# Performance work log

Hardware: AMD Instinct MI355X
Metric: run time of the kernel (lower is better)

The kernel has to match this reference:

```python
import jax, jax.numpy as jnp
import numpy as np

ALPHA = 0.01
BETA = 3e-05
OUT_H, OUT_W = 256, 256
KSIZE, SIGMA = 5, 4.0


def _gaussian_kernel2d(ks=KSIZE, sigma=SIGMA):
    x = jnp.arange(ks, dtype=jnp.float32) - (ks - 1) / 2.0
    g = jnp.exp(-(x * x) / (2.0 * sigma * sigma))
    g = g / g.sum()
    return jnp.outer(g, g)  # [ks, ks]


def _gaussian_blur(maps):
    # maps: [B, H, W]; reflect padding + depthwise 5x5 gaussian (kornia-style GaussianBlur2d)
    k = _gaussian_kernel2d()[None, None]  # [1,1,5,5]
    p = KSIZE // 2
    x = jnp.pad(maps[:, None], ((0, 0), (0, 0), (p, p), (p, p)), mode='reflect')
    y = jax.lax.conv_general_dilated(x, k, (1, 1), 'VALID')
    return y[:, 0]


def _resize_bilinear_align_corners(x, oh, ow):
    # x: [B, h, w] -> [B, oh, ow], torch F.interpolate(mode='bilinear', align_corners=True)
    B, h, w = x.shape
    ys = jnp.linspace(0.0, h - 1.0, oh)
    xs = jnp.linspace(0.0, w - 1.0, ow)
    y0 = jnp.floor(ys).astype(jnp.int32)
    x0 = jnp.floor(xs).astype(jnp.int32)
    y1 = jnp.minimum(y0 + 1, h - 1)
    x1 = jnp.minimum(x0 + 1, w - 1)
    fy = (ys - y0.astype(ys.dtype))[:, None]  # [oh,1]
    fx = (xs - x0.astype(xs.dtype))[None, :]  # [1,ow]
    a = x[:, y0][:, :, x0]
    b = x[:, y0][:, :, x1]
    c = x[:, y1][:, :, x0]
    d = x[:, y1][:, :, x1]
    top = a * (1.0 - fx) + b * fx
    bot = c * (1.0 - fx) + d * fx
    return top * (1.0 - fy) + bot * fy


def setup_inputs() -> dict:
    key = jax.random.key(0)
    k0, k1, k2 = jax.random.split(key, 3)
    B = 256
    return {
        'out0': jax.random.normal(k0, (B, 64, 64), jnp.float32),
        'out1': jax.random.normal(k1, (B, 32, 32), jnp.float32),
        'out2': jax.random.normal(k2, (B, 16, 16), jnp.float32),
    }


def reference(out0, out1, out2):
    outputs = [out0, out1, out2]
    B = out0.shape[0]
    # per-sample max of each scale -> softmax-weighted selection of per-sample weight
    max_vals = jnp.stack([o.reshape(B, -1).max(axis=1) for o in outputs], axis=1)  # [B,3]
    probs = jax.nn.softmax(max_vals, axis=1)
    mask = probs > probs.mean(axis=1, keepdims=True)  # probs > prob_mean
    cnt = mask.sum(axis=1)
    sel_mean = (max_vals * mask).sum(axis=1) / jnp.maximum(cnt, 1)
    total_weights = jnp.where(cnt > 0, jnp.maximum(sel_mean * ALPHA, BETA), BETA)  # [B]
    # multi-scale fusion: bilinear(align_corners=True) upsample to (256,256) and sum
    maps = _resize_bilinear_align_corners(out0, OUT_H, OUT_W)
    maps = maps + _resize_bilinear_align_corners(out1, OUT_H, OUT_W)
    maps = maps + _resize_bilinear_align_corners(out2, OUT_H, OUT_W)
    # gaussian blur then per-sample score. torch takes topk(k=f(total_weights)).values[0],
    # and topk values are sorted descending, so values[0] == max (k / total_weights drop out).
    blurred = _gaussian_blur(maps)
    scores = blurred.reshape(B, -1).max(axis=1)
    del total_weights  # only influenced the (unused) top-k size in the original
    return scores[:, None], maps
```

## Files before the change

kernel.cpp:

```cpp
#include <hip/hip_runtime.h>
#include <math.h>


static constexpr int W  = 256;
static constexpr int QH = 4;
static constexpr int ROWS = 64;

__device__ __forceinline__ int reflect256(int i) {
    if (i < 0) i = -i;
    if (i > 255) i = 510 - i;
    return i;
}

template<int H>
__device__ __forceinline__ float sample_direct(const float* __restrict__ base,
                                               int ry, int x0, int x1, float fx) {
    int   iy = ry * (H - 1);
    int   y0 = iy / 255;
    float fy = (float)(iy - 255 * y0) * (1.0f / 255.0f);
    int   y1 = min(y0 + 1, H - 1);
    float a = base[y0 * H + x0];
    float b = base[y0 * H + x1];
    float c = base[y1 * H + x0];
    float d = base[y1 * H + x1];
    float top = a + fx * (b - a);
    float bot = c + fx * (d - c);
    return top + fy * (bot - top);
}

__global__ __launch_bounds__(256, 4) void fused_kernel(
    const float* __restrict__ in0,
    const float* __restrict__ in1,
    const float* __restrict__ in2,
    float* __restrict__ part,
    float* __restrict__ maps)
{
    const int t   = threadIdx.x;
    const int bid = blockIdx.x;
    const int b   = bid >> 2;
    const int r0  = (bid & 3) * ROWS;

    __shared__ float s0[64 * 64];
    __shared__ float s1[32 * 32];
    __shared__ float s2[16 * 16];
    __shared__ float vsm[16][W];
    __shared__ float red[4];

    {
        const float4* g0 = (const float4*)(in0 + (size_t)b * 4096);
        const float4* g1 = (const float4*)(in1 + (size_t)b * 1024);
        const float4* g2 = (const float4*)(in2 + (size_t)b * 256);
        float4* l0 = (float4*)s0;
        float4* l1 = (float4*)s1;
        float4* l2 = (float4*)s2;
#pragma unroll
        for (int i = 0; i < 4; ++i) l0[t + i * 256] = g0[t + i * 256];
        l1[t] = g1[t];
        if (t < 64) l2[t] = g2[t];
    }
    __syncthreads();

    const float inv255 = 1.0f / 255.0f;
    int ix0 = t * 63; int x00 = ix0 / 255; float fx0 = (float)(ix0 - 255 * x00) * inv255; int x01 = min(x00 + 1, 63);
    int ix1 = t * 31; int x10 = ix1 / 255; float fx1 = (float)(ix1 - 255 * x10) * inv255; int x11 = min(x10 + 1, 31);
    int ix2 = t * 15; int x20 = ix2 / 255; float fx2 = (float)(ix2 - 255 * x20) * inv255; int x21 = min(x20 + 1, 15);

    auto xr0 = [&](int y) { float a = s0[y * 64 + x00]; float bb = s0[y * 64 + x01]; return a + fx0 * (bb - a); };
    auto xr1 = [&](int y) { float a = s1[y * 32 + x10]; float bb = s1[y * 32 + x11]; return a + fx1 * (bb - a); };
    auto xr2 = [&](int y) { float a = s2[y * 16 + x20]; float bb = s2[y * 16 + x21]; return a + fx2 * (bb - a); };

    auto direct = [&](int rn) -> float {
        int ry = reflect256(rn);
        return sample_direct<64>(s0, ry, x00, x01, fx0)
             + sample_direct<32>(s1, ry, x10, x11, fx1)
             + sample_direct<16>(s2, ry, x20, x21, fx2);
    };

    const float e1 = expf(-1.0f / 32.0f);
    const float e2 = expf(-4.0f / 32.0f);
    const float nrm = 1.0f + 2.0f * e1 + 2.0f * e2;
    const float wc = 1.0f / nrm, wa = e1 / nrm, wb = e2 / nrm;

    float m0 = direct(r0 - 2);
    float m1 = direct(r0 - 1);
    float m2 = direct(r0);
    float m3 = direct(r0 + 1);
    float* __restrict__ mbase = maps + ((size_t)b * W) * W + t;
    mbase[(size_t)(r0) * W]     = m2;
    mbase[(size_t)(r0 + 1) * W] = m3;

    int iy;
    iy = (r0 + 2) * 63; int ya = iy / 255; int rem0 = iy - ya * 255;
    float rlo0 = xr0(ya), rhi0 = xr0(min(ya + 1, 63));
    iy = (r0 + 2) * 31; int yb = iy / 255; int rem1 = iy - yb * 255;
    float rlo1 = xr1(yb), rhi1 = xr1(min(yb + 1, 31));
    iy = (r0 + 2) * 15; int yc = iy / 255; int rem2 = iy - yc * 255;
    float rlo2 = xr2(yc), rhi2 = xr2(min(yc + 1, 15));

    const int qx = t & 63;
    const int c0 = qx * 4;
    const int rowbase = t >> 6;
    const int ca = max(c0 - 4, 0);
    const int cc = min(c0 + 4, 252);

    float gmax = -INFINITY;

    for (int i = 0; i < ROWS; ++i) {
        const int rn = r0 + 2 + i;
        float mnew;
        if (rn <= 255) {
            float v0 = rlo0 + (float)rem0 * inv255 * (rhi0 - rlo0);
            float v1 = rlo1 + (float)rem1 * inv255 * (rhi1 - rlo1);
            float v2 = rlo2 + (float)rem2 * inv255 * (rhi2 - rlo2);
            mnew = v0 + v1 + v2;
            rem0 += 63; if (rem0 >= 255) { rem0 -= 255; ya++; rlo0 = rhi0; rhi0 = xr0(min(ya + 1, 63)); }
            rem1 += 31; if (rem1 >= 255) { rem1 -= 255; yb++; rlo1 = rhi1; rhi1 = xr1(min(yb + 1, 31)); }
            rem2 += 15; if (rem2 >= 255) { rem2 -= 255; yc++; rlo2 = rhi2; rhi2 = xr2(min(yc + 1, 15)); }
        } else {
            mnew = direct(rn);
        }

        if (i < ROWS - 2) {
            mbase[(size_t)rn * W] = mnew;
        }

        vsm[i & 15][t] = wb * (m0 + mnew) + wa * (m1 + m3) + wc * m2;
        m0 = m1; m1 = m2; m2 = m3; m3 = mnew;

        if ((i & 15) == 15) {
            __syncthreads();
#pragma unroll
            for (int k = 0; k < 4; ++k) {
                const int row = rowbase + k * 4;
                const float4 Bv = *(const float4*)&vsm[row][c0];
                const float4 Av = *(const float4*)&vsm[row][ca];
                const float4 Cv = *(const float4*)&vsm[row][cc];
                const float a2 = (qx == 0)  ? Bv.z : Av.z;
                const float a3 = (qx == 0)  ? Bv.y : Av.w;
                const float c4 = (qx == 63) ? Bv.z : Cv.x;
                const float c5 = (qx == 63) ? Bv.y : Cv.y;
                float o0 = wc * Bv.x + wa * (a3 + Bv.y)   + wb * (a2 + Bv.z);
                float o1 = wc * Bv.y + wa * (Bv.x + Bv.z) + wb * (a3 + Bv.w);
                float o2 = wc * Bv.z + wa * (Bv.y + Bv.w) + wb * (Bv.x + c4);
                float o3 = wc * Bv.w + wa * (Bv.z + c4)   + wb * (Bv.y + c5);
                gmax = fmaxf(gmax, fmaxf(fmaxf(o0, o1), fmaxf(o2, o3)));
            }
            __syncthreads();
        }
    }

#pragma unroll
    for (int off = 32; off > 0; off >>= 1)
        gmax = fmaxf(gmax, __shfl_down(gmax, off));
    if ((t & 63) == 0) red[t >> 6] = gmax;
    __syncthreads();
    if (t == 0)
        part[bid] = fmaxf(fmaxf(red[0], red[1]), fmaxf(red[2], red[3]));
}

__global__ void reduce_kernel(const float* __restrict__ part,
                              float* __restrict__ scores, int B) {
    int i = blockIdx.x * blockDim.x + threadIdx.x;
    if (i < B) {
        float m = part[QH * i];
#pragma unroll
        for (int k = 1; k < QH; ++k) m = fmaxf(m, part[QH * i + k]);
        scores[i] = m;
    }
}

extern "C" void kernel_launch(void* const* d_in, const int* in_sizes, int n_in,
                              void* d_out, int out_size, void* d_ws, size_t ws_size,
                              hipStream_t stream) {
    const float* in0 = (const float*)d_in[0];
    const float* in1 = (const float*)d_in[1];
    const float* in2 = (const float*)d_in[2];
    const int B = in_sizes[0] / (64 * 64);

    float* scores = (float*)d_out;
    float* maps   = (float*)d_out + B;
    float* part   = (float*)d_ws;

    hipLaunchKernelGGL(fused_kernel, dim3(B * QH), dim3(256), 0, stream,
                       in0, in1, in2, part, maps);
    hipLaunchKernelGGL(reduce_kernel, dim3((B + 255) / 256), dim3(256), 0, stream,
                       part, scores, B);
}
```

Baseline: 100.4 us.

## Give each wavefront a 16-row strip with 4 columns per lane and shuffle-based blur

Re-partitions work so each wavefront handles 16 output rows and each lane computes 4 adjacent columns, writing maps with float4 stores. The horizontal blur pass now uses wavefront shuffles instead of a shared-memory staging buffer with block-wide barriers, which removes the vsm array and the __syncthreads inside the row loop. In exchange, each wavefront recomputes 4 halo rows directly, and each lane holds several 4-wide register arrays, which raises register pressure.

```diff
diff --git a/kernel.cpp b/kernel.cpp
--- a/kernel.cpp
+++ b/kernel.cpp
@@ -4,28 +4,11 @@
 
 static constexpr int W  = 256;
 static constexpr int QH = 4;
-static constexpr int ROWS = 64;
 
 __device__ __forceinline__ int reflect256(int i) {
     if (i < 0) i = -i;
     if (i > 255) i = 510 - i;
     return i;
-}
-
-template<int H>
-__device__ __forceinline__ float sample_direct(const float* __restrict__ base,
-                                               int ry, int x0, int x1, float fx) {
-    int   iy = ry * (H - 1);
-    int   y0 = iy / 255;
-    float fy = (float)(iy - 255 * y0) * (1.0f / 255.0f);
-    int   y1 = min(y0 + 1, H - 1);
-    float a = base[y0 * H + x0];
-    float b = base[y0 * H + x1];
-    float c = base[y1 * H + x0];
-    float d = base[y1 * H + x1];
-    float top = a + fx * (b - a);
-    float bot = c + fx * (d - c);
-    return top + fy * (bot - top);
 }
 
 __global__ __launch_bounds__(256, 4) void fused_kernel(
@@ -36,14 +19,17 @@
     float* __restrict__ maps)
 {
     const int t   = threadIdx.x;
+    const int q   = t & 63;
+    const int wv  = __builtin_amdgcn_readfirstlane(t >> 6);
     const int bid = blockIdx.x;
     const int b   = bid >> 2;
-    const int r0  = (bid & 3) * ROWS;
+    const int r0  = (bid & 3) * 64;
+    const int rw0 = r0 + wv * 16;
+    const int c0  = q * 4;
 
     __shared__ float s0[64 * 64];
     __shared__ float s1[32 * 32];
     __shared__ float s2[16 * 16];
-    __shared__ float vsm[16][W];
     __shared__ float red[4];
 
     {
@@ -61,98 +47,165 @@
     __syncthreads();
 
     const float inv255 = 1.0f / 255.0f;
-    int ix0 = t * 63; int x00 = ix0 / 255; float fx0 = (float)(ix0 - 255 * x00) * inv255; int x01 = min(x00 + 1, 63);
-    int ix1 = t * 31; int x10 = ix1 / 255; float fx1 = (float)(ix1 - 255 * x10) * inv255; int x11 = min(x10 + 1, 31);
-    int ix2 = t * 15; int x20 = ix2 / 255; float fx2 = (float)(ix2 - 255 * x20) * inv255; int x21 = min(x20 + 1, 15);
-
-    auto xr0 = [&](int y) { float a = s0[y * 64 + x00]; float bb = s0[y * 64 + x01]; return a + fx0 * (bb - a); };
-    auto xr1 = [&](int y) { float a = s1[y * 32 + x10]; float bb = s1[y * 32 + x11]; return a + fx1 * (bb - a); };
-    auto xr2 = [&](int y) { float a = s2[y * 16 + x20]; float bb = s2[y * 16 + x21]; return a + fx2 * (bb - a); };
-
-    auto direct = [&](int rn) -> float {
-        int ry = reflect256(rn);
-        return sample_direct<64>(s0, ry, x00, x01, fx0)
-             + sample_direct<32>(s1, ry, x10, x11, fx1)
-             + sample_direct<16>(s2, ry, x20, x21, fx2);
+    int x00[4]; float fx0[4];
+    int x10[4]; float fx1[4];
+    int x20[4]; float fx2[4];
+#pragma unroll
+    for (int k = 0; k < 4; ++k) {
+        const int c = c0 + k;
+        int ix = c * 63; x00[k] = ix / 255; fx0[k] = (float)(ix - 255 * x00[k]) * inv255;
+        ix = c * 31;     x10[k] = ix / 255; fx1[k] = (float)(ix - 255 * x10[k]) * inv255;
+        ix = c * 15;     x20[k] = ix / 255; fx2[k] = (float)(ix - 255 * x20[k]) * inv255;
+    }
+
+    auto xq0 = [&](int y, float* o) {
+        const float* row = s0 + y * 64;
+#pragma unroll
+        for (int k = 0; k < 4; ++k) {
+            int xa = x00[k], xb = min(xa + 1, 63);
+            float a = row[xa], bb = row[xb];
+            o[k] = a + fx0[k] * (bb - a);
+        }
+    };
+    auto xq1 = [&](int y, float* o) {
+        const float* row = s1 + y * 32;
+#pragma unroll
+        for (int k = 0; k < 4; ++k) {
+            int xa = x10[k], xb = min(xa + 1, 31);
+            float a = row[xa], bb = row[xb];
+            o[k] = a + fx1[k] * (bb - a);
+        }
+    };
+    auto xq2 = [&](int y, float* o) {
+        const float* row = s2 + y * 16;
+#pragma unroll
+        for (int k = 0; k < 4; ++k) {
+            int xa = x20[k], xb = min(xa + 1, 15);
+            float a = row[xa], bb = row[xb];
+            o[k] = a + fx2[k] * (bb - a);
+        }
+    };
+
+    auto direct4 = [&](int rn, float* o) {
+        const int ry = reflect256(rn);
+        int iy0 = ry * 63; int ya0 = iy0 / 255; float fya = (float)(iy0 - 255 * ya0) * inv255; int ya1 = min(ya0 + 1, 63);
+        int iy1 = ry * 31; int yb0 = iy1 / 255; float fyb = (float)(iy1 - 255 * yb0) * inv255; int yb1 = min(yb0 + 1, 31);
+        int iy2 = ry * 15; int yc0 = iy2 / 255; float fyc = (float)(iy2 - 255 * yc0) * inv255; int yc1 = min(yc0 + 1, 15);
+        const float* r0a = s0 + ya0 * 64; const float* r0b = s0 + ya1 * 64;
+        const float* r1a = s1 + yb0 * 32; const float* r1b = s1 + yb1 * 32;
+        const float* r2a = s2 + yc0 * 16; const float* r2b = s2 + yc1 * 16;
+#pragma unroll
+        for (int k = 0; k < 4; ++k) {
+            int xa = x00[k], xb = min(xa + 1, 63);
+            float a = r0a[xa], bv = r0a[xb], cv = r0b[xa], dv = r0b[xb];
+            float top = a + fx0[k] * (bv - a);
+            float bot = cv + fx0[k] * (dv - cv);
+            float v = top + fya * (bot - top);
+            xa = x10[k]; xb = min(xa + 1, 31);
+            a = r1a[xa]; bv = r1a[xb]; cv = r1b[xa]; dv = r1b[xb];
+            top = a + fx1[k] * (bv - a);
+            bot = cv + fx1[k] * (dv - cv);
+            v += top + fyb * (bot - top);
+            xa = x20[k]; xb = min(xa + 1, 15);
+            a = r2a[xa]; bv = r2a[xb]; cv = r2b[xa]; dv = r2b[xb];
+            top = a + fx2[k] * (bv - a);
+            bot = cv + fx2[k] * (dv - cv);
+            v += top + fyc * (bot - top);
+            o[k] = v;
+        }
     };
 
     const float e1 = expf(-1.0f / 32.0f);
     const float e2 = expf(-4.0f / 32.0f);
     const float nrm = 1.0f + 2.0f * e1 + 2.0f * e2;
-    const float wc = 1.0f / nrm, wa = e1 / nrm, wb = e2 / nrm;
-
-    float m0 = direct(r0 - 2);
-    float m1 = direct(r0 - 1);
-    float m2 = direct(r0);
-    float m3 = direct(r0 + 1);
-    float* __restrict__ mbase = maps + ((size_t)b * W) * W + t;
-    mbase[(size_t)(r0) * W]     = m2;
-    mbase[(size_t)(r0 + 1) * W] = m3;
-
-    int iy;
-    iy = (r0 + 2) * 63; int ya = iy / 255; int rem0 = iy - ya * 255;
-    float rlo0 = xr0(ya), rhi0 = xr0(min(ya + 1, 63));
-    iy = (r0 + 2) * 31; int yb = iy / 255; int rem1 = iy - yb * 255;
-    float rlo1 = xr1(yb), rhi1 = xr1(min(yb + 1, 31));
-    iy = (r0 + 2) * 15; int yc = iy / 255; int rem2 = iy - yc * 255;
-    float rlo2 = xr2(yc), rhi2 = xr2(min(yc + 1, 15));
-
-    const int qx = t & 63;
-    const int c0 = qx * 4;
-    const int rowbase = t >> 6;
-    const int ca = max(c0 - 4, 0);
-    const int cc = min(c0 + 4, 252);
+    const float gwc = 1.0f / nrm, gwa = e1 / nrm, gwb = e2 / nrm;
+
+    float m0[4], m1[4], m2[4], m3[4], mn[4];
+    direct4(rw0 - 2, m0);
+    direct4(rw0 - 1, m1);
+    direct4(rw0,     m2);
+    direct4(rw0 + 1, m3);
+
+    float* __restrict__ mpr = maps + ((size_t)b * W + (size_t)rw0) * W + c0;
+    *(float4*)(mpr)     = make_float4(m2[0], m2[1], m2[2], m2[3]);
+    *(float4*)(mpr + W) = make_float4(m3[0], m3[1], m3[2], m3[3]);
+
+    int iy, ya, yb, yc, rem0, rem1, rem2;
+    float rlo0[4], rhi0[4], rlo1[4], rhi1[4], rlo2[4], rhi2[4];
+    iy = (rw0 + 2) * 63; ya = iy / 255; rem0 = iy - 255 * ya; xq0(ya, rlo0); xq0(min(ya + 1, 63), rhi0);
+    iy = (rw0 + 2) * 31; yb = iy / 255; rem1 = iy - 255 * yb; xq1(yb, rlo1); xq1(min(yb + 1, 31), rhi1);
+    iy = (rw0 + 2) * 15; yc = iy / 255; rem2 = iy - 255 * yc; xq2(yc, rlo2); xq2(min(yc + 1, 15), rhi2);
 
     float gmax = -INFINITY;
 
-    for (int i = 0; i < ROWS; ++i) {
-        const int rn = r0 + 2 + i;
-        float mnew;
+#pragma unroll 4
+    for (int i = 0; i < 16; ++i) {
+        const int rn = rw0 + 2 + i;
         if (rn <= 255) {
-            float v0 = rlo0 + (float)rem0 * inv255 * (rhi0 - rlo0);
-            float v1 = rlo1 + (float)rem1 * inv255 * (rhi1 - rlo1);
-            float v2 = rlo2 + (float)rem2 * inv255 * (rhi2 - rlo2);
-            mnew = v0 + v1 + v2;
-            rem0 += 63; if (rem0 >= 255) { rem0 -= 255; ya++; rlo0 = rhi0; rhi0 = xr0(min(ya + 1, 63)); }
-            rem1 += 31; if (rem1 >= 255) { rem1 -= 255; yb++; rlo1 = rhi1; rhi1 = xr1(min(yb + 1, 31)); }
-            rem2 += 15; if (rem2 >= 255) { rem2 -= 255; yc++; rlo2 = rhi2; rhi2 = xr2(min(yc + 1, 15)); }
+            const float w0 = (float)rem0 * inv255;
+            const float w1 = (float)rem1 * inv255;
+            const float w2 = (float)rem2 * inv255;
+#pragma unroll
+            for (int k = 0; k < 4; ++k) {
+                float v0 = rlo0[k] + w0 * (rhi0[k] - rlo0[k]);
+                float v1 = rlo1[k] + w1 * (rhi1[k] - rlo1[k]);
+                float v2 = rlo2[k] + w2 * (rhi2[k] - rlo2[k]);
+                mn[k] = v0 + v1 + v2;
+            }
+            rem0 += 63;
+            if (rem0 >= 255) {
+                rem0 -= 255; ++ya;
+#pragma unroll
+                for (int k = 0; k < 4; ++k) rlo0[k] = rhi0[k];
+                xq0(min(ya + 1, 63), rhi0);
+            }
+            rem1 += 31;
+            if (rem1 >= 255) {
+                rem1 -= 255; ++yb;
+#pragma unroll
+                for (int k = 0; k < 4; ++k) rlo1[k] = rhi1[k];
+                xq1(min(yb + 1, 31), rhi1);
+            }
+            rem2 += 15;
+            if (rem2 >= 255) {
+                rem2 -= 255; ++yc;
+#pragma unroll
+                for (int k = 0; k < 4; ++k) rlo2[k] = rhi2[k];
+                xq2(min(yc + 1, 15), rhi2);
+            }
         } else {
-            mnew = direct(rn);
-        }
-
-        if (i < ROWS - 2) {
-            mbase[(size_t)rn * W] = mnew;
-        }
-
-        vsm[i & 15][t] = wb * (m0 + mnew) + wa * (m1 + m3) + wc * m2;
-        m0 = m1; m1 = m2; m2 = m3; m3 = mnew;
-
-        if ((i & 15) == 15) {
-            __syncthreads();
-#pragma unroll
-            for (int k = 0; k < 4; ++k) {
-                const int row = rowbase + k * 4;
-                const float4 Bv = *(const float4*)&vsm[row][c0];
-                const float4 Av = *(const float4*)&vsm[row][ca];
-                const float4 Cv = *(const float4*)&vsm[row][cc];
-                const float a2 = (qx == 0)  ? Bv.z : Av.z;
-                const float a3 = (qx == 0)  ? Bv.y : Av.w;
-                const float c4 = (qx == 63) ? Bv.z : Cv.x;
-                const float c5 = (qx == 63) ? Bv.y : Cv.y;
-                float o0 = wc * Bv.x + wa * (a3 + Bv.y)   + wb * (a2 + Bv.z);
-                float o1 = wc * Bv.y + wa * (Bv.x + Bv.z) + wb * (a3 + Bv.w);
-                float o2 = wc * Bv.z + wa * (Bv.y + Bv.w) + wb * (Bv.x + c4);
-                float o3 = wc * Bv.w + wa * (Bv.z + c4)   + wb * (Bv.y + c5);
-                gmax = fmaxf(gmax, fmaxf(fmaxf(o0, o1), fmaxf(o2, o3)));
-            }
-            __syncthreads();
-        }
+            direct4(rn, mn);
+        }
+
+        if (i < 14)
+            *(float4*)(mpr + (size_t)(2 + i) * W) = make_float4(mn[0], mn[1], mn[2], mn[3]);
+
+        float vr0 = gwb * (m0[0] + mn[0]) + gwa * (m1[0] + m3[0]) + gwc * m2[0];
+        float vr1 = gwb * (m0[1] + mn[1]) + gwa * (m1[1] + m3[1]) + gwc * m2[1];
+        float vr2 = gwb * (m0[2] + mn[2]) + gwa * (m1[2] + m3[2]) + gwc * m2[2];
+        float vr3 = gwb * (m0[3] + mn[3]) + gwa * (m1[3] + m3[3]) + gwc * m2[3];
+#pragma unroll
+        for (int k = 0; k < 4; ++k) { m0[k] = m1[k]; m1[k] = m2[k]; m2[k] = m3[k]; m3[k] = mn[k]; }
+
+        float az = __shfl_up(vr2, 1);
+        float aw = __shfl_up(vr3, 1);
+        float cx = __shfl_down(vr0, 1);
+        float cy = __shfl_down(vr1, 1);
+        float a2 = (q == 0)  ? vr2 : az;
+        float a3 = (q == 0)  ? vr1 : aw;
+        float c4 = (q == 63) ? vr2 : cx;
+        float c5 = (q == 63) ? vr1 : cy;
+        float o0 = gwc * vr0 + gwa * (a3 + vr1)  + gwb * (a2 + vr2);
+        float o1 = gwc * vr1 + gwa * (vr0 + vr2) + gwb * (a3 + vr3);
+        float o2 = gwc * vr2 + gwa * (vr1 + vr3) + gwb * (vr0 + c4);
+        float o3 = gwc * vr3 + gwa * (vr2 + c4)  + gwb * (vr1 + c5);
+        gmax = fmaxf(gmax, fmaxf(fmaxf(o0, o1), fmaxf(o2, o3)));
     }
 
 #pragma unroll
     for (int off = 32; off > 0; off >>= 1)
         gmax = fmaxf(gmax, __shfl_down(gmax, off));
-    if ((t & 63) == 0) red[t >> 6] = gmax;
+    if (q == 0) red[wv] = gmax;
     __syncthreads();
     if (t == 0)
         part[bid] = fmaxf(fmaxf(red[0], red[1]), fmaxf(red[2], red[3]));
```

New measurement: 109.4 us. +8.9%, slower.
